# Kernel tuning notes

Measured on AMD Instinct MI355X. Metric: run time of the kernel, lower is better.

The kernel has to match this reference:

```python
import jax, jax.numpy as jnp
import numpy as np

N_CHANNELS = 22
N_PATCHES = 64
N_NODES = N_CHANNELS * N_PATCHES  # 1408
EMBED_DIM = 256
N_HEADS = 4
HEAD_DIM = EMBED_DIM // N_HEADS
ALPHA = 0.15
TOP_P = 0.85
DIST_THRESH = 0.55
BATCH = 16

TCP_PAIRS = [('FP1','F7'),('F7','T3'),('T3','T5'),('T5','O1'),('FP2','F8'),('F8','T4'),('T4','T6'),('T6','O2'),('FP1','F3'),('F3','C3'),('C3','P3'),('P3','O1'),('FP2','F4'),('F4','C4'),('C4','P4'),('P4','O2'),('A1','T3'),('T3','C3'),('C3','CZ'),('CZ','C4'),('C4','T4'),('T4','A2')]
_ELECTRODE_3D = {'FP1':(-0.31,0.95,0.0),'FP2':(0.31,0.95,0.0),'F7':(-0.81,0.59,0.0),'F3':(-0.55,0.67,0.5),'FZ':(0.0,0.71,0.71),'F4':(0.55,0.67,0.5),'F8':(0.81,0.59,0.0),'T3':(-1.0,0.0,0.0),'C3':(-0.57,0.0,0.82),'CZ':(0.0,0.0,1.0),'C4':(0.57,0.0,0.82),'T4':(1.0,0.0,0.0),'T5':(-0.81,-0.59,0.0),'P3':(-0.55,-0.67,0.5),'PZ':(0.0,-0.71,0.71),'P4':(0.55,-0.67,0.5),'T6':(0.81,-0.59,0.0),'O1':(-0.31,-0.95,0.0),'O2':(0.31,-0.95,0.0),'A1':(-1.05,0.0,-0.3),'A2':(1.05,0.0,-0.3)}


def _build_masks():
    # channel positions = midpoint of each bipolar TCP pair -> [22,3]
    ch_pos = np.array([(np.array(_ELECTRODE_3D[a]) + np.array(_ELECTRODE_3D[b])) / 2.0 for a, b in TCP_PAIRS])
    d = np.linalg.norm(ch_pos[:, None, :] - ch_pos[None, :, :], axis=-1)
    ch_adj = (d < DIST_THRESH).astype(np.float32)
    np.fill_diagonal(ch_adj, 0.0)
    # node = ch * n_patches + t ; spatial edges only between same t: kron(ch_adj, I_P)
    spatial = np.kron(ch_adj, np.eye(N_PATCHES, dtype=np.float32))
    # temporal: same channel, |p - p'| == 1
    T = np.zeros((N_PATCHES, N_PATCHES), dtype=np.float32)
    idx = np.arange(N_PATCHES - 1)
    T[idx, idx + 1] = 1.0
    T[idx + 1, idx] = 1.0
    temporal = np.kron(np.eye(N_CHANNELS, dtype=np.float32), T)
    return jnp.asarray(temporal), jnp.asarray(spatial)


def setup_inputs() -> dict:
    key = jax.random.key(0)
    ks = jax.random.split(key, 8)
    D, H, HD = EMBED_DIM, N_HEADS, HEAD_DIM
    s = 1.0 / np.sqrt(D)
    x = jax.random.normal(ks[0], (BATCH, N_NODES, D), dtype=jnp.float32)
    proj_w = jax.random.uniform(ks[1], (H, HD, D), jnp.float32, -s, s)
    gate_w = jax.random.uniform(ks[2], (3, D), jnp.float32, -s, s)
    gate_b = jax.random.uniform(ks[3], (3,), jnp.float32, -s, s)
    score_w1 = jax.random.uniform(ks[4], (D // 2, D), jnp.float32, -s, s)
    score_b1 = jax.random.uniform(ks[5], (D // 2,), jnp.float32, -s, s)
    s2 = 1.0 / np.sqrt(D // 2)
    score_w2 = jax.random.uniform(ks[6], (1, D // 2), jnp.float32, -s2, s2)
    score_b2 = jax.random.uniform(ks[7], (1,), jnp.float32, -s2, s2)
    threshold = jnp.asarray(0.5, dtype=jnp.float32)
    temporal_mask, spatial_mask = _build_masks()
    return {"x": x, "proj_w": proj_w, "gate_w": gate_w, "gate_b": gate_b,
            "score_w1": score_w1, "score_b1": score_b1, "score_w2": score_w2,
            "score_b2": score_b2, "threshold": threshold,
            "temporal_mask": temporal_mask, "spatial_mask": spatial_mask}


def _safe_dist(d2):
    d2 = jnp.maximum(d2, 0.0)
    return jnp.where(d2 > 0, jnp.sqrt(jnp.where(d2 > 0, d2, 1.0)), 0.0)


def reference(x, proj_w, gate_w, gate_b, score_w1, score_b1, score_w2, score_b2,
              threshold, temporal_mask, spatial_mask):
    B, N, D = x.shape
    H = proj_w.shape[0]
    k = max(1, int(N * ALPHA))
    b_idx = jnp.arange(B)[:, None, None]
    r_idx = jnp.arange(N)[None, :, None]

    # ---- MultiHeadDistanceKNN: mean over heads of (knn-mask * gaussian sim) ----
    adj = jnp.zeros((B, N, N), x.dtype)
    for h in range(H):
        z = x @ proj_w[h].T                                  # [B,N,hd]
        sq = jnp.sum(z * z, axis=-1)                         # [B,N]
        d2 = sq[:, :, None] + sq[:, None, :] - 2.0 * jnp.einsum('bnd,bmd->bnm', z, z)
        dist = _safe_dist(d2)                                # [B,N,N]
        _, topk_idx = jax.lax.top_k(-dist, k)                # k smallest dists
        m = jnp.zeros((B, N, N), x.dtype).at[b_idx, r_idx, topk_idx].set(1.0)
        m = jnp.maximum(m, jnp.swapaxes(m, -1, -2))          # symmetrize
        sim = jnp.exp(-dist * dist / (2.0 * jnp.mean(dist) ** 2 + 1e-8))
        adj = adj + sim * m
    adj = adj / H

    # ---- Temporal / Spatial filters (fixed masks) ----
    adj_t = adj * temporal_mask[None]
    adj_s = adj * spatial_mask[None]

    # ---- Pathological filter: MLP node score -> outer product -> soft gate ----
    h1 = jax.nn.gelu(x @ score_w1.T + score_b1, approximate=False)
    scores = jax.nn.sigmoid((h1 @ score_w2.T + score_b2)[..., 0])    # [B,N]
    edge_w = scores[:, :, None] * scores[:, None, :]
    adj_p = adj * jax.nn.sigmoid((edge_w - threshold) * 10.0)

    # ---- NoisyGatedRouter (eval: no noise): softmax -> top-p truncate -> renorm ----
    probs = jax.nn.softmax(x @ gate_w.T + gate_b, axis=-1)           # [B,N,3]
    order = jnp.argsort(-probs, axis=-1)
    sp = jnp.take_along_axis(probs, order, axis=-1)
    keep = (jnp.cumsum(sp, axis=-1) - sp) < TOP_P
    sp = sp * keep.astype(sp.dtype)
    inv = jnp.argsort(order, axis=-1)
    w = jnp.take_along_axis(sp, inv, axis=-1)                        # scatter back
    w = w / (jnp.sum(w, axis=-1, keepdims=True) + 1e-8)              # [B,N,3]

    # ---- Mix filters with per-edge weights (w_i + w_j)/2 ----
    out = jnp.zeros_like(adj)
    for f, a in enumerate((adj_t, adj_s, adj_p)):
        wf = w[:, :, f]
        ewf = (wf[:, :, None] + wf[:, None, :]) * 0.5
        out = out + a * ewf
    return out
```

## Files before the change

kernel.cpp:

```cpp
#include <hip/hip_runtime.h>
#include <math.h>

typedef __attribute__((ext_vector_type(8))) short bf16x8;
typedef __attribute__((ext_vector_type(4))) float f32x4;

__device__ __forceinline__ float wsum64(float v) {
#pragma unroll
  for (int d = 32; d > 0; d >>= 1) v += __shfl_xor(v, d, 64);
  return v;
}

__device__ __forceinline__ unsigned short f2bf(float f) {
  unsigned u = __float_as_uint(f);
  u = (u + 0x7FFFu + ((u >> 16) & 1u)) >> 16;
  return (unsigned short)u;
}

__global__ void k_init(const float* __restrict__ smask, float* __restrict__ chadj,
                       double* __restrict__ sums) {
  int t = threadIdx.x;
  if (t < 4) sums[t] = 0.0;
  if (t < 484) {
    int c1 = t / 22, c2 = t % 22;
    chadj[t] = smask[(size_t)(c1 * 64) * 1408 + (size_t)c2 * 64];
  }
}

__global__ __launch_bounds__(256) void k_gemm_in(
    const float* __restrict__ x, const float* __restrict__ projw,
    const float* __restrict__ w1, float* __restrict__ z, float* __restrict__ zT,
    unsigned short* __restrict__ zb, float* __restrict__ h1) {
  __shared__ float xs[16][68];
  __shared__ float wsT[16][68];
  __shared__ float ldsT[64][65];
  int n0 = blockIdx.x * 64;
  int o0 = blockIdx.y * 64;
  int tid = threadIdx.x;
  int tx = tid & 15, ty = tid >> 4;
  float acc[4][4];
#pragma unroll
  for (int i = 0; i < 4; i++)
#pragma unroll
    for (int j = 0; j < 4; j++) acc[i][j] = 0.f;
  for (int kc = 0; kc < 16; kc++) {
#pragma unroll
    for (int rep = 0; rep < 4; rep++) {
      int e = tid + rep * 256;
      int n = e >> 4, k = e & 15;
      xs[k][n] = x[(size_t)(n0 + n) * 256 + kc * 16 + k];
      int row = o0 + n;
      wsT[k][n] = (row < 256) ? projw[(size_t)row * 256 + kc * 16 + k]
                              : w1[(size_t)(row - 256) * 256 + kc * 16 + k];
    }
    __syncthreads();
#pragma unroll
    for (int k = 0; k < 16; k++) {
      float4 a4 = *(const float4*)&xs[k][4 * ty];
      float4 w4 = *(const float4*)&wsT[k][4 * tx];
      float ar[4] = {a4.x, a4.y, a4.z, a4.w};
      float wr[4] = {w4.x, w4.y, w4.z, w4.w};
#pragma unroll
      for (int i = 0; i < 4; i++)
#pragma unroll
        for (int j = 0; j < 4; j++) acc[i][j] = fmaf(ar[i], wr[j], acc[i][j]);
    }
    __syncthreads();
  }
  if (blockIdx.y >= 4) {
#pragma unroll
    for (int i = 0; i < 4; i++) {
      size_t base = (size_t)(n0 + 4 * ty + i) * 128 + (o0 - 256) + 4 * tx;
      float4 t;
      t.x = acc[i][0]; t.y = acc[i][1]; t.z = acc[i][2]; t.w = acc[i][3];
      *(float4*)&h1[base] = t;
    }
  } else {
#pragma unroll
    for (int i = 0; i < 4; i++) {
      size_t base = (size_t)(n0 + 4 * ty + i) * 256 + o0 + 4 * tx;
      float4 t;
      t.x = acc[i][0]; t.y = acc[i][1]; t.z = acc[i][2]; t.w = acc[i][3];
      *(float4*)&z[base] = t;
      unsigned lo = (unsigned)f2bf(acc[i][0]) | ((unsigned)f2bf(acc[i][1]) << 16);
      unsigned hi = (unsigned)f2bf(acc[i][2]) | ((unsigned)f2bf(acc[i][3]) << 16);
      uint2 u2; u2.x = lo; u2.y = hi;
      *(uint2*)(zb + base) = u2;
    }
    __syncthreads();
#pragma unroll
    for (int i = 0; i < 4; i++)
#pragma unroll
      for (int j = 0; j < 4; j++) ldsT[4 * tx + j][4 * ty + i] = acc[i][j];
    __syncthreads();
    int bblk = blockIdx.x / 22;
    int nbase = (blockIdx.x % 22) * 64;
#pragma unroll
    for (int rep = 0; rep < 16; rep++) {
      int e = tid + rep * 256;
      int oo = e >> 6, nn = e & 63;
      zT[(size_t)((bblk * 4 + blockIdx.y) * 64 + oo) * 1408 + nbase + nn] = ldsT[oo][nn];
    }
  }
}

__global__ __launch_bounds__(256) void k_node(
    const float* __restrict__ x, const float* __restrict__ z,
    const float* __restrict__ h1, const float* __restrict__ gw,
    const float* __restrict__ gb, const float* __restrict__ b1,
    const float* __restrict__ w2, const float* __restrict__ b2v,
    float* __restrict__ sq, float4* __restrict__ wnode) {
  int tid = threadIdx.x;
  int w = tid >> 6, lane = tid & 63;
  int node = blockIdx.x * 4 + w;
  int b = node / 1408, n = node % 1408;
  const float* zr = z + (size_t)node * 256;
  const float* xr = x + (size_t)node * 256;
#pragma unroll
  for (int c = 0; c < 4; c++) {
    float val = zr[c * 64 + lane];
    float s = wsum64(val * val);
    if (lane == 0) sq[(size_t)(b * 4 + c) * 1408 + n] = s;
  }
  float gl[3];
#pragma unroll
  for (int f = 0; f < 3; f++) {
    float p = 0.f;
#pragma unroll
    for (int c = 0; c < 4; c++)
      p = fmaf(xr[c * 64 + lane], gw[f * 256 + c * 64 + lane], p);
    gl[f] = wsum64(p) + gb[f];
  }
  const float* hr = h1 + (size_t)node * 128;
  float ps = 0.f;
#pragma unroll
  for (int c = 0; c < 2; c++) {
    float t = hr[c * 64 + lane] + b1[c * 64 + lane];
    float g = 0.5f * t * (1.f + erff(t * 0.7071067811865475f));
    ps = fmaf(g, w2[c * 64 + lane], ps);
  }
  float sc = wsum64(ps) + b2v[0];
  sc = 1.f / (1.f + expf(-sc));
  float mx = fmaxf(gl[0], fmaxf(gl[1], gl[2]));
  float ex[3];
  float esum = 0.f;
#pragma unroll
  for (int f = 0; f < 3; f++) { ex[f] = expf(gl[f] - mx); esum += ex[f]; }
  float p3[3];
#pragma unroll
  for (int f = 0; f < 3; f++) p3[f] = ex[f] / esum;
  int rk[3];
#pragma unroll
  for (int f = 0; f < 3; f++) {
    int r = 0;
#pragma unroll
    for (int g = 0; g < 3; g++)
      r += ((p3[g] > p3[f]) || (p3[g] == p3[f] && g < f)) ? 1 : 0;
    rk[f] = r;
  }
  float sp[3]; int oi[3];
#pragma unroll
  for (int f = 0; f < 3; f++) { sp[rk[f]] = p3[f]; oi[rk[f]] = f; }
  bool k1 = sp[0] < 0.85f;
  bool k2 = (sp[0] + sp[1]) < 0.85f;
  float wv[3];
  wv[oi[0]] = sp[0];
  wv[oi[1]] = k1 ? sp[1] : 0.f;
  wv[oi[2]] = k2 ? sp[2] : 0.f;
  float inv = 1.f / (wv[0] + wv[1] + wv[2] + 1e-8f);
  if (lane == 0) wnode[node] = make_float4(wv[0] * inv, wv[1] * inv, wv[2] * inv, sc);
}

template <int TC>
__device__ __forceinline__ void dotstrip16(float (&v)[16][6],
                                           const float* __restrict__ zTh,
                                           const float (&As)[64][16], int jb) {
#pragma unroll
  for (int r = 0; r < 16; r++)
#pragma unroll
    for (int t = 0; t < TC; t++) v[r][t] = 0.f;
  const float* bp = zTh + jb;
  float bc[TC];
#pragma unroll
  for (int t = 0; t < TC; t++) bc[t] = bp[t * 64];
  const float* pn = bp + 1408;
#pragma unroll 1
  for (int k = 0; k < 63; k++) {
    float bn[TC];
#pragma unroll
    for (int t = 0; t < TC; t++) bn[t] = pn[t * 64];
    pn += 1408;
    float4 a0 = *(const float4*)&As[k][0];
    float4 a1 = *(const float4*)&As[k][4];
    float4 a2 = *(const float4*)&As[k][8];
    float4 a3 = *(const float4*)&As[k][12];
    float ar[16] = {a0.x, a0.y, a0.z, a0.w, a1.x, a1.y, a1.z, a1.w,
                    a2.x, a2.y, a2.z, a2.w, a3.x, a3.y, a3.z, a3.w};
#pragma unroll
    for (int r = 0; r < 16; r++)
#pragma unroll
      for (int t = 0; t < TC; t++) v[r][t] = fmaf(ar[r], bc[t], v[r][t]);
#pragma unroll
    for (int t = 0; t < TC; t++) bc[t] = bn[t];
  }
  {
    float4 a0 = *(const float4*)&As[63][0];
    float4 a1 = *(const float4*)&As[63][4];
    float4 a2 = *(const float4*)&As[63][8];
    float4 a3 = *(const float4*)&As[63][12];
    float ar[16] = {a0.x, a0.y, a0.z, a0.w, a1.x, a1.y, a1.z, a1.w,
                    a2.x, a2.y, a2.z, a2.w, a3.x, a3.y, a3.z, a3.w};
#pragma unroll
    for (int r = 0; r < 16; r++)
#pragma unroll
      for (int t = 0; t < TC; t++) v[r][t] = fmaf(ar[r], bc[t], v[r][t]);
  }
}

__global__ __launch_bounds__(256, 3) void k_pass1(
    const float* __restrict__ zT, const float* __restrict__ sq,
    unsigned* __restrict__ bm, double* __restrict__ sums) {
  __shared__ float As[64][16];
  __shared__ float srowL[16];
  __shared__ unsigned hist[8][528];
  __shared__ float cand[16][128];
  __shared__ unsigned candCnt[16];
  __shared__ int tbinS[16], rstarS[16];
  __shared__ float TS[16];
  int b = blockIdx.y, h = blockIdx.z;
  int i0 = blockIdx.x * 16;
  int tid = threadIdx.x;
  int w = tid >> 6, lane = tid & 63;
  const float* zTh = zT + (size_t)((b * 4 + h) * 64) * 1408;
  const float* sqh = sq + (size_t)(b * 4 + h) * 1408;
#pragma unroll
  for (int rep = 0; rep < 4; rep++) {
    int e = tid + rep * 256;
    int k = e >> 4, r = e & 15;
    As[k][r] = zTh[(size_t)k * 1408 + i0 + r];
  }
  if (tid < 16) srowL[tid] = sqh[i0 + tid];
  {
    unsigned* histF = &hist[0][0];
    for (int u = tid; u < 8 * 528; u += 256) histF[u] = 0u;
  }
  if (tid < 16) candCnt[tid] = 0u;
  __syncthreads();

  const int TC = (w < 2) ? 6 : 5;
  const int tbase = (w < 2) ? 6 * w : 5 * w + 2;
  int jb = tbase * 64 + lane;
  float sqj[6];
#pragma unroll
  for (int t = 0; t < 6; t++)
    sqj[t] = (t < 5 || TC == 6) ? sqh[jb + t * 64] : 0.f;

  float v[16][6];
  if (w < 2) dotstrip16<6>(v, zTh, As, jb);
  else       dotstrip16<5>(v, zTh, As, jb);

  float ssum = 0.f;
#pragma unroll
  for (int r = 0; r < 16; r++) {
    float sr = srowL[r];
#pragma unroll
    for (int t = 0; t < 6; t++) {
      if (t < 5 || TC == 6) {
        float d = sr + sqj[t] - 2.f * v[r][t];
        d = fmaxf(d, 0.f);
        ssum += sqrtf(d);
        v[r][t] = d;
        unsigned key = (unsigned)fminf(d * 4.0f, 511.0f);
        atomicAdd(&hist[r >> 1][key + (key >> 6)], 1u << ((r & 1) * 16));
      }
    }
  }
  __syncthreads();

#pragma unroll 1
  for (int q = 0; q < 4; q++) {
    int r = 4 * w + q;
    int sh = (r & 1) * 16;
    const unsigned* hrow = hist[r >> 1];
    unsigned partial = 0;
#pragma unroll
    for (int u = 0; u < 8; u++) {
      int bin = 8 * lane + u;
      partial += (hrow[bin + (bin >> 6)] >> sh) & 0xffffu;
    }
    unsigned inc = partial;
#pragma unroll
    for (int d = 1; d < 64; d <<= 1) {
      unsigned u2 = __shfl_up(inc, d, 64);
      if (lane >= d) inc += u2;
    }
    unsigned long long mk = __ballot(inc >= 211u);
    int Ls = __ffsll(mk) - 1;
    unsigned cbefore = (Ls > 0) ? (unsigned)__shfl((int)inc, Ls - 1, 64) : 0u;
    int tb = -1;
    unsigned run = cbefore, cbelow = cbefore;
#pragma unroll
    for (int u = 0; u < 8; u++) {
      int bin = 8 * Ls + u;
      unsigned c = (hrow[bin + (bin >> 6)] >> sh) & 0xffffu;
      if (tb < 0) {
        if (run + c >= 211u) { tb = bin; cbelow = run; }
        run += c;
      }
    }
    if (lane == 0) { tbinS[r] = tb; rstarS[r] = 211 - (int)cbelow; }
  }
  __syncthreads();

#pragma unroll
  for (int r = 0; r < 16; r++) {
    int tb = tbinS[r];
#pragma unroll
    for (int t = 0; t < 6; t++) {
      if (t < 5 || TC == 6) {
        float d = v[r][t];
        unsigned key = (unsigned)fminf(d * 4.0f, 511.0f);
        if ((int)key == tb) {
          unsigned id = atomicAdd(&candCnt[r], 1u);
          if (id < 128u) cand[r][id] = d;
        }
      }
    }
  }
  __syncthreads();

#pragma unroll 1
  for (int q = 0; q < 4; q++) {
    int r = 4 * w + q;
    int rstar = rstarS[r];
    unsigned craw = candCnt[r];
    int cnt = (craw > 128u) ? 128 : (int)craw;
    float t2l = INFINITY;
    for (int base = 0; base < cnt; base += 64) {
      int ci = base + lane;
      if (ci < cnt) {
        float xm = cand[r][ci];
        int below = 0, eq = 0;
        for (int m = 0; m < cnt; m++) {
          float y = cand[r][m];
          below += (y < xm) ? 1 : 0;
          eq += (y == xm) ? 1 : 0;
        }
        if (below < rstar && rstar <= below + eq) t2l = fminf(t2l, xm);
      }
    }
#pragma unroll
    for (int dd = 32; dd > 0; dd >>= 1) t2l = fminf(t2l, __shfl_xor(t2l, dd, 64));
    if (lane == 0) TS[r] = t2l;
  }
  __syncthreads();

#pragma unroll
  for (int r = 0; r < 16; r++) {
    float T = TS[r];
    unsigned* bmrow = bm + (size_t)((h * 16 + b) * 1408 + i0 + r) * 44;
#pragma unroll
    for (int t = 0; t < 6; t++) {
      if (t < 5 || TC == 6) {
        unsigned long long bl = __ballot(v[r][t] <= T);
        int tile = tbase + t;
        if (lane == 0) bmrow[tile * 2] = (unsigned)bl;
        if (lane == 32) bmrow[tile * 2 + 1] = (unsigned)(bl >> 32);
      }
    }
  }
  ssum = wsum64(ssum);
  if (lane == 0) atomicAdd(&sums[h], (double)ssum);
}

__global__ __launch_bounds__(256) void k_final(
    const unsigned short* __restrict__ zb, const float* __restrict__ sq,
    const float4* __restrict__ wnode, const unsigned* __restrict__ bm,
    const double* __restrict__ sums, const float* __restrict__ chadj,
    const float* __restrict__ thrp, float* __restrict__ out) {
  int it = blockIdx.x, jt = blockIdx.y, b = blockIdx.z;
  int tid = threadIdx.x, wv = tid >> 6, lane = tid & 63;
  int quad = lane >> 4, l15 = lane & 15;
  float c2h[4];
#pragma unroll
  for (int h = 0; h < 4; h++) {
    double mu = sums[h] * (1.0 / (16.0 * 1408.0 * 1408.0));
    c2h[h] = (float)(1.0 / (2.0 * mu * mu + 1e-8)) * 1.44269504088896f;
  }
  float thr = thrp[0];
  int ib = it * 64 + wv * 16;
  const unsigned short* za = zb + (size_t)(b * 1408 + ib + l15) * 256;
  bf16x8 af[4][2];
#pragma unroll
  for (int h = 0; h < 4; h++)
#pragma unroll
    for (int k0 = 0; k0 < 2; k0++)
      af[h][k0] = *(const bf16x8*)(za + h * 64 + k0 * 32 + quad * 8);
  int ibq = ib + quad * 4;
  float4 wi[4];
  float sqi[4][4];
#pragma unroll
  for (int reg = 0; reg < 4; reg++) {
    int i = ibq + reg;
    wi[reg] = wnode[b * 1408 + i];
#pragma unroll
    for (int h = 0; h < 4; h++) sqi[reg][h] = sq[(size_t)(b * 4 + h) * 1408 + i];
  }
#pragma unroll
  for (int js = 0; js < 4; js++) {
    int j = jt * 64 + js * 16 + l15;
    const unsigned short* zj = zb + (size_t)(b * 1408 + j) * 256;
    f32x4 acc[4];
#pragma unroll
    for (int h = 0; h < 4; h++) {
      bf16x8 b0 = *(const bf16x8*)(zj + h * 64 + quad * 8);
      bf16x8 b1f = *(const bf16x8*)(zj + h * 64 + 32 + quad * 8);
      f32x4 a = {0.f, 0.f, 0.f, 0.f};
      a = __builtin_amdgcn_mfma_f32_16x16x32_bf16(af[h][0], b0, a, 0, 0, 0);
      a = __builtin_amdgcn_mfma_f32_16x16x32_bf16(af[h][1], b1f, a, 0, 0, 0);
      acc[h] = a;
    }
    float sqj[4];
#pragma unroll
    for (int h = 0; h < 4; h++) sqj[h] = sq[(size_t)(b * 4 + h) * 1408 + j];
    float4 wj = wnode[b * 1408 + j];
    float adjv[4] = {0.f, 0.f, 0.f, 0.f};
#pragma unroll
    for (int h = 0; h < 4; h++) {
      const unsigned* bmh = bm + (size_t)(h * 16 + b) * 1408 * 44;
      unsigned wJ = bmh[(size_t)j * 44 + (ibq >> 5)];
#pragma unroll
      for (int reg = 0; reg < 4; reg++) {
        int i = ibq + reg;
        float d2 = sqi[reg][h] + sqj[h] - 2.f * acc[h][reg];
        d2 = fmaxf(d2, 0.f);
        float sim = exp2f(-d2 * c2h[h]);
        unsigned bi = bmh[(size_t)i * 44 + (j >> 5)] >> (j & 31);
        unsigned bj = wJ >> (i & 31);
        adjv[reg] += (((bi | bj) & 1u) != 0u) ? sim : 0.f;
      }
    }
#pragma unroll
    for (int reg = 0; reg < 4; reg++) {
      int i = ibq + reg;
      int chi = i >> 6, pi = i & 63, chj = j >> 6, pj = j & 63;
      float e0 = 0.5f * (wi[reg].x + wj.x);
      float e1 = 0.5f * (wi[reg].y + wj.y);
      float e2 = 0.5f * (wi[reg].z + wj.z);
      float a2 = 0.f;
      if (chi == chj) {
        int dp = pi - pj;
        if (dp == 1 || dp == -1) a2 += e0;
      }
      if (pi == pj && chadj[chi * 22 + chj] != 0.f) a2 += e1;
      float xw = (wi[reg].w * wj.w - thr) * 10.f;
      float pt = 1.f / (1.f + exp2f(-xw * 1.44269504088896f));
      a2 += pt * e2;
      out[(size_t)(b * 1408 + i) * 1408 + j] = 0.25f * adjv[reg] * a2;
    }
  }
}

extern "C" void kernel_launch(void* const* d_in, const int* in_sizes, int n_in,
                              void* d_out, int out_size, void* d_ws, size_t ws_size,
                              hipStream_t stream) {
  (void)in_sizes; (void)n_in; (void)out_size; (void)ws_size;
  const float* x = (const float*)d_in[0];
  const float* projw = (const float*)d_in[1];
  const float* gw = (const float*)d_in[2];
  const float* gb = (const float*)d_in[3];
  const float* w1 = (const float*)d_in[4];
  const float* b1 = (const float*)d_in[5];
  const float* w2 = (const float*)d_in[6];
  const float* b2 = (const float*)d_in[7];
  const float* thr = (const float*)d_in[8];
  const float* smask = (const float*)d_in[10];
  float* out = (float*)d_out;
  char* ws = (char*)d_ws;
  size_t off = 0;
  auto take = [&](size_t bytes) {
    char* p = ws + off;
    off += (bytes + 255) & ~(size_t)255;
    return p;
  };
  float* z = (float*)take((size_t)22528 * 256 * 4);
  float* zT = (float*)take((size_t)22528 * 256 * 4);
  unsigned short* zb = (unsigned short*)take((size_t)22528 * 256 * 2);
  float* h1 = (float*)take((size_t)22528 * 128 * 4);
  float* sq = (float*)take((size_t)16 * 4 * 1408 * 4);
  float4* wnode = (float4*)take((size_t)22528 * 16);
  unsigned* bm = (unsigned*)take((size_t)4 * 16 * 1408 * 44 * 4);
  float* chadj = (float*)take(484 * 4);
  double* sums = (double*)take(4 * 8);

  hipLaunchKernelGGL(k_init, dim3(1), dim3(512), 0, stream, smask, chadj, sums);
  hipLaunchKernelGGL(k_gemm_in, dim3(352, 6), dim3(256), 0, stream, x, projw, w1,
                     z, zT, zb, h1);
  hipLaunchKernelGGL(k_node, dim3(5632), dim3(256), 0, stream, x, z, h1, gw, gb,
                     b1, w2, b2, sq, wnode);
  hipLaunchKernelGGL(k_pass1, dim3(88, 16, 4), dim3(256), 0, stream, zT, sq, bm,
                     sums);
  hipLaunchKernelGGL(k_final, dim3(22, 22, 16), dim3(256), 0, stream, zb, sq,
                     wnode, bm, sums, chadj, thr, out);
}
```

Baseline: 917.4 us.

## Split pass1 row strip into two 8-row halves to cut registers

The pass1 kernel now processes its 16-row block as two sequential halves of 8 rows. Each half recomputes the dot-product strip, histogram, threshold selection and bitmask writes. This halves the per-thread accumulator array and the shared histogram and candidate buffers, lowering register and LDS pressure so more blocks can run per CU. The cost is that the global z column loads are read twice and there are more barriers per block.

New measurement: 988.8 us. +7.8%, slower.

```diff
diff --git a/kernel.cpp b/kernel.cpp
--- a/kernel.cpp
+++ b/kernel.cpp
@@ -171,11 +171,12 @@
 }
 
 template <int TC>
-__device__ __forceinline__ void dotstrip16(float (&v)[16][6],
-                                           const float* __restrict__ zTh,
-                                           const float (&As)[64][16], int jb) {
-#pragma unroll
-  for (int r = 0; r < 16; r++)
+__device__ __forceinline__ void dotstrip8(float (&v)[8][6],
+                                          const float* __restrict__ zTh,
+                                          const float (&As)[64][16], int jb,
+                                          int rbase) {
+#pragma unroll
+  for (int r = 0; r < 8; r++)
 #pragma unroll
     for (int t = 0; t < TC; t++) v[r][t] = 0.f;
   const float* bp = zTh + jb;
@@ -189,28 +190,22 @@
 #pragma unroll
     for (int t = 0; t < TC; t++) bn[t] = pn[t * 64];
     pn += 1408;
-    float4 a0 = *(const float4*)&As[k][0];
-    float4 a1 = *(const float4*)&As[k][4];
-    float4 a2 = *(const float4*)&As[k][8];
-    float4 a3 = *(const float4*)&As[k][12];
-    float ar[16] = {a0.x, a0.y, a0.z, a0.w, a1.x, a1.y, a1.z, a1.w,
-                    a2.x, a2.y, a2.z, a2.w, a3.x, a3.y, a3.z, a3.w};
-#pragma unroll
-    for (int r = 0; r < 16; r++)
+    float4 a0 = *(const float4*)&As[k][rbase];
+    float4 a1 = *(const float4*)&As[k][rbase + 4];
+    float ar[8] = {a0.x, a0.y, a0.z, a0.w, a1.x, a1.y, a1.z, a1.w};
+#pragma unroll
+    for (int r = 0; r < 8; r++)
 #pragma unroll
       for (int t = 0; t < TC; t++) v[r][t] = fmaf(ar[r], bc[t], v[r][t]);
 #pragma unroll
     for (int t = 0; t < TC; t++) bc[t] = bn[t];
   }
   {
-    float4 a0 = *(const float4*)&As[63][0];
-    float4 a1 = *(const float4*)&As[63][4];
-    float4 a2 = *(const float4*)&As[63][8];
-    float4 a3 = *(const float4*)&As[63][12];
-    float ar[16] = {a0.x, a0.y, a0.z, a0.w, a1.x, a1.y, a1.z, a1.w,
-                    a2.x, a2.y, a2.z, a2.w, a3.x, a3.y, a3.z, a3.w};
-#pragma unroll
-    for (int r = 0; r < 16; r++)
+    float4 a0 = *(const float4*)&As[63][rbase];
+    float4 a1 = *(const float4*)&As[63][rbase + 4];
+    float ar[8] = {a0.x, a0.y, a0.z, a0.w, a1.x, a1.y, a1.z, a1.w};
+#pragma unroll
+    for (int r = 0; r < 8; r++)
 #pragma unroll
       for (int t = 0; t < TC; t++) v[r][t] = fmaf(ar[r], bc[t], v[r][t]);
   }
@@ -221,11 +216,11 @@
     unsigned* __restrict__ bm, double* __restrict__ sums) {
   __shared__ float As[64][16];
   __shared__ float srowL[16];
-  __shared__ unsigned hist[8][528];
-  __shared__ float cand[16][128];
-  __shared__ unsigned candCnt[16];
-  __shared__ int tbinS[16], rstarS[16];
-  __shared__ float TS[16];
+  __shared__ unsigned hist[4][528];
+  __shared__ float cand[8][128];
+  __shared__ unsigned candCnt[8];
+  __shared__ int tbinS[8], rstarS[8];
+  __shared__ float TS[8];
   int b = blockIdx.y, h = blockIdx.z;
   int i0 = blockIdx.x * 16;
   int tid = threadIdx.x;
@@ -239,11 +234,6 @@
     As[k][r] = zTh[(size_t)k * 1408 + i0 + r];
   }
   if (tid < 16) srowL[tid] = sqh[i0 + tid];
-  {
-    unsigned* histF = &hist[0][0];
-    for (int u = tid; u < 8 * 528; u += 256) histF[u] = 0u;
-  }
-  if (tid < 16) candCnt[tid] = 0u;
   __syncthreads();
 
   const int TC = (w < 2) ? 6 : 5;
@@ -254,117 +244,128 @@
   for (int t = 0; t < 6; t++)
     sqj[t] = (t < 5 || TC == 6) ? sqh[jb + t * 64] : 0.f;
 
-  float v[16][6];
-  if (w < 2) dotstrip16<6>(v, zTh, As, jb);
-  else       dotstrip16<5>(v, zTh, As, jb);
-
   float ssum = 0.f;
-#pragma unroll
-  for (int r = 0; r < 16; r++) {
-    float sr = srowL[r];
-#pragma unroll
-    for (int t = 0; t < 6; t++) {
-      if (t < 5 || TC == 6) {
-        float d = sr + sqj[t] - 2.f * v[r][t];
-        d = fmaxf(d, 0.f);
-        ssum += sqrtf(d);
-        v[r][t] = d;
-        unsigned key = (unsigned)fminf(d * 4.0f, 511.0f);
-        atomicAdd(&hist[r >> 1][key + (key >> 6)], 1u << ((r & 1) * 16));
-      }
-    }
-  }
-  __syncthreads();
-
 #pragma unroll 1
-  for (int q = 0; q < 4; q++) {
-    int r = 4 * w + q;
-    int sh = (r & 1) * 16;
-    const unsigned* hrow = hist[r >> 1];
-    unsigned partial = 0;
-#pragma unroll
-    for (int u = 0; u < 8; u++) {
-      int bin = 8 * lane + u;
-      partial += (hrow[bin + (bin >> 6)] >> sh) & 0xffffu;
-    }
-    unsigned inc = partial;
-#pragma unroll
-    for (int d = 1; d < 64; d <<= 1) {
-      unsigned u2 = __shfl_up(inc, d, 64);
-      if (lane >= d) inc += u2;
-    }
-    unsigned long long mk = __ballot(inc >= 211u);
-    int Ls = __ffsll(mk) - 1;
-    unsigned cbefore = (Ls > 0) ? (unsigned)__shfl((int)inc, Ls - 1, 64) : 0u;
-    int tb = -1;
-    unsigned run = cbefore, cbelow = cbefore;
-#pragma unroll
-    for (int u = 0; u < 8; u++) {
-      int bin = 8 * Ls + u;
-      unsigned c = (hrow[bin + (bin >> 6)] >> sh) & 0xffffu;
-      if (tb < 0) {
-        if (run + c >= 211u) { tb = bin; cbelow = run; }
-        run += c;
-      }
-    }
-    if (lane == 0) { tbinS[r] = tb; rstarS[r] = 211 - (int)cbelow; }
-  }
-  __syncthreads();
-
-#pragma unroll
-  for (int r = 0; r < 16; r++) {
-    int tb = tbinS[r];
-#pragma unroll
-    for (int t = 0; t < 6; t++) {
-      if (t < 5 || TC == 6) {
-        float d = v[r][t];
-        unsigned key = (unsigned)fminf(d * 4.0f, 511.0f);
-        if ((int)key == tb) {
-          unsigned id = atomicAdd(&candCnt[r], 1u);
-          if (id < 128u) cand[r][id] = d;
+  for (int half = 0; half < 2; half++) {
+    const int rbase = half * 8;
+    float v[8][6];
+    if (w < 2) dotstrip8<6>(v, zTh, As, jb, rbase);
+    else       dotstrip8<5>(v, zTh, As, jb, rbase);
+
+    {
+      unsigned* histF = &hist[0][0];
+      for (int u = tid; u < 4 * 528; u += 256) histF[u] = 0u;
+    }
+    if (tid < 8) candCnt[tid] = 0u;
+    __syncthreads();
+
+#pragma unroll
+    for (int r = 0; r < 8; r++) {
+      float sr = srowL[rbase + r];
+#pragma unroll
+      for (int t = 0; t < 6; t++) {
+        if (t < 5 || TC == 6) {
+          float d = sr + sqj[t] - 2.f * v[r][t];
+          d = fmaxf(d, 0.f);
+          ssum += sqrtf(d);
+          v[r][t] = d;
+          unsigned key = (unsigned)fminf(d * 4.0f, 511.0f);
+          atomicAdd(&hist[r >> 1][key + (key >> 6)], 1u << ((r & 1) * 16));
         }
       }
     }
-  }
-  __syncthreads();
+    __syncthreads();
 
 #pragma unroll 1
-  for (int q = 0; q < 4; q++) {
-    int r = 4 * w + q;
-    int rstar = rstarS[r];
-    unsigned craw = candCnt[r];
-    int cnt = (craw > 128u) ? 128 : (int)craw;
-    float t2l = INFINITY;
-    for (int base = 0; base < cnt; base += 64) {
-      int ci = base + lane;
-      if (ci < cnt) {
-        float xm = cand[r][ci];
-        int below = 0, eq = 0;
-        for (int m = 0; m < cnt; m++) {
-          float y = cand[r][m];
-          below += (y < xm) ? 1 : 0;
-          eq += (y == xm) ? 1 : 0;
+    for (int q = 0; q < 2; q++) {
+      int r = 2 * w + q;
+      int sh = (r & 1) * 16;
+      const unsigned* hrow = hist[r >> 1];
+      unsigned partial = 0;
+#pragma unroll
+      for (int u = 0; u < 8; u++) {
+        int bin = 8 * lane + u;
+        partial += (hrow[bin + (bin >> 6)] >> sh) & 0xffffu;
+      }
+      unsigned inc = partial;
+#pragma unroll
+      for (int d = 1; d < 64; d <<= 1) {
+        unsigned u2 = __shfl_up(inc, d, 64);
+        if (lane >= d) inc += u2;
+      }
+      unsigned long long mk = __ballot(inc >= 211u);
+      int Ls = __ffsll(mk) - 1;
+      unsigned cbefore = (Ls > 0) ? (unsigned)__shfl((int)inc, Ls - 1, 64) : 0u;
+      int tb = -1;
+      unsigned run = cbefore, cbelow = cbefore;
+#pragma unroll
+      for (int u = 0; u < 8; u++) {
+        int bin = 8 * Ls + u;
+        unsigned c = (hrow[bin + (bin >> 6)] >> sh) & 0xffffu;
+        if (tb < 0) {
+          if (run + c >= 211u) { tb = bin; cbelow = run; }
+          run += c;
         }
-        if (below < rstar && rstar <= below + eq) t2l = fminf(t2l, xm);
-      }
-    }
-#pragma unroll
-    for (int dd = 32; dd > 0; dd >>= 1) t2l = fminf(t2l, __shfl_xor(t2l, dd, 64));
-    if (lane == 0) TS[r] = t2l;
-  }
-  __syncthreads();
-
-#pragma unroll
-  for (int r = 0; r < 16; r++) {
-    float T = TS[r];
-    unsigned* bmrow = bm + (size_t)((h * 16 + b) * 1408 + i0 + r) * 44;
-#pragma unroll
-    for (int t = 0; t < 6; t++) {
-      if (t < 5 || TC == 6) {
-        unsigned long long bl = __ballot(v[r][t] <= T);
-        int tile = tbase + t;
-        if (lane == 0) bmrow[tile * 2] = (unsigned)bl;
-        if (lane == 32) bmrow[tile * 2 + 1] = (unsigned)(bl >> 32);
+      }
+      if (lane == 0) { tbinS[r] = tb; rstarS[r] = 211 - (int)cbelow; }
+    }
+    __syncthreads();
+
+#pragma unroll
+    for (int r = 0; r < 8; r++) {
+      int tb = tbinS[r];
+#pragma unroll
+      for (int t = 0; t < 6; t++) {
+        if (t < 5 || TC == 6) {
+          float d = v[r][t];
+          unsigned key = (unsigned)fminf(d * 4.0f, 511.0f);
+          if ((int)key == tb) {
+            unsigned id = atomicAdd(&candCnt[r], 1u);
+            if (id < 128u) cand[r][id] = d;
+          }
+        }
+      }
+    }
+    __syncthreads();
+
+#pragma unroll 1
+    for (int q = 0; q < 2; q++) {
+      int r = 2 * w + q;
+      int rstar = rstarS[r];
+      unsigned craw = candCnt[r];
+      int cnt = (craw > 128u) ? 128 : (int)craw;
+      float t2l = INFINITY;
+      for (int base = 0; base < cnt; base += 64) {
+        int ci = base + lane;
+        if (ci < cnt) {
+          float xm = cand[r][ci];
+          int below = 0, eq = 0;
+          for (int m = 0; m < cnt; m++) {
+            float y = cand[r][m];
+            below += (y < xm) ? 1 : 0;
+            eq += (y == xm) ? 1 : 0;
+          }
+          if (below < rstar && rstar <= below + eq) t2l = fminf(t2l, xm);
+        }
+      }
+#pragma unroll
+      for (int dd = 32; dd > 0; dd >>= 1) t2l = fminf(t2l, __shfl_xor(t2l, dd, 64));
+      if (lane == 0) TS[r] = t2l;
+    }
+    __syncthreads();
+
+#pragma unroll
+    for (int r = 0; r < 8; r++) {
+      float T = TS[r];
+      unsigned* bmrow = bm + (size_t)((h * 16 + b) * 1408 + i0 + rbase + r) * 44;
+#pragma unroll
+      for (int t = 0; t < 6; t++) {
+        if (t < 5 || TC == 6) {
+          unsigned long long bl = __ballot(v[r][t] <= T);
+          int tile = tbase + t;
+          if (lane == 0) bmrow[tile * 2] = (unsigned)bl;
+          if (lane == 32) bmrow[tile * 2 + 1] = (unsigned)(bl >> 32);
+        }
       }
     }
   }
```
